# Optimization experiments

Measured on AMD Instinct MI355X. Metric: run time of the kernel, lower is better.

The kernel has to match this reference:

```python
import jax, jax.numpy as jnp
import numpy as np

N, E, G, L = 50000, 800000, 512, 4
DIN, D = 128, 64


def setup_inputs() -> dict:
    key = jax.random.key(0)
    ks = jax.random.split(key, 32)
    s = 0.1  # weight scale
    inp = {
        "nodes_feat": jax.random.normal(ks[0], (N, DIN), jnp.float32),
        "edges_feat": jax.random.normal(ks[1], (E, 1), jnp.float32),
        "nodes_num_norm_sqrt": jax.random.uniform(ks[2], (N, 1), jnp.float32),
        "edges_num_norm_sqrt": jax.random.uniform(ks[3], (E, 1), jnp.float32),
        "W_h": jax.random.normal(ks[4], (DIN, D), jnp.float32) * s,
        "b_h": jax.random.normal(ks[5], (D,), jnp.float32) * s,
        "W_e": jax.random.normal(ks[6], (1, D), jnp.float32) * s,
        "b_e": jax.random.normal(ks[7], (D,), jnp.float32) * s,
        "Wa": jax.random.normal(ks[8], (L, D, D), jnp.float32) * s,
        "ba": jax.random.normal(ks[9], (L, D), jnp.float32) * s,
        "Wb": jax.random.normal(ks[10], (L, D, D), jnp.float32) * s,
        "bb": jax.random.normal(ks[11], (L, D), jnp.float32) * s,
        "Wc": jax.random.normal(ks[12], (L, D, D), jnp.float32) * s,
        "bc": jax.random.normal(ks[13], (L, D), jnp.float32) * s,
        "Wd": jax.random.normal(ks[14], (L, D, D), jnp.float32) * s,
        "bd": jax.random.normal(ks[15], (L, D), jnp.float32) * s,
        "We": jax.random.normal(ks[16], (L, D, D), jnp.float32) * s,
        "be": jax.random.normal(ks[17], (L, D), jnp.float32) * s,
        "gamma_h": jnp.ones((L, D), jnp.float32),
        "beta_h": jnp.zeros((L, D), jnp.float32),
        "gamma_e": jnp.ones((L, D), jnp.float32),
        "beta_e": jnp.zeros((L, D), jnp.float32),
        "edge_src": jax.random.randint(ks[18], (E,), 0, N, jnp.int32),
        "edge_dst": jax.random.randint(ks[19], (E,), 0, N, jnp.int32),
        "node_graph_ids": jnp.sort(jax.random.randint(ks[20], (N,), 0, G, jnp.int32)),
        "num_graphs": G,
    }
    return inp


def _bn(x, gamma, beta):
    # BatchNorm1d, training mode (biased batch statistics)
    mu = jnp.mean(x, axis=0)
    var = jnp.var(x, axis=0)
    return gamma * (x - mu) * jax.lax.rsqrt(var + 1e-5) + beta


def reference(nodes_feat, edges_feat, nodes_num_norm_sqrt, edges_num_norm_sqrt,
              W_h, b_h, W_e, b_e,
              Wa, ba, Wb, bb, Wc, bc, Wd, bd, We, be,
              gamma_h, beta_h, gamma_e, beta_e,
              edge_src, edge_dst, node_graph_ids, num_graphs):
    seg = jax.ops.segment_sum
    n_nodes = nodes_feat.shape[0]
    h = nodes_feat @ W_h + b_h          # [N, D]
    e = edges_feat @ W_e + b_e          # [E, D]
    for l in range(Wa.shape[0]):
        h_in, e_in = h, e
        Ah = h @ Wa[l] + ba[l]
        Bh = h @ Wb[l] + bb[l]
        Dh = h @ Wd[l] + bd[l]
        Eh = h @ We[l] + be[l]
        e_new = (e @ Wc[l] + bc[l]) + Dh[edge_src] + Eh[edge_dst]   # [E, D]
        sigma = jax.nn.sigmoid(e_new)
        num = seg(sigma * Bh[edge_src], edge_dst, num_segments=n_nodes)
        den = seg(sigma, edge_dst, num_segments=n_nodes)
        h_new = Ah + num / (den + 1e-6)
        h_new = h_new * nodes_num_norm_sqrt      # graph norm
        e_new = e_new * edges_num_norm_sqrt
        h_new = jax.nn.relu(_bn(h_new, gamma_h[l], beta_h[l]))
        e_new = jax.nn.relu(_bn(e_new, gamma_e[l], beta_e[l]))
        h = h_in + h_new                          # residual
        e = e_in + e_new
    # dgl.mean_nodes: segment mean of node features per graph
    ones = jnp.ones((n_nodes, 1), h.dtype)
    counts = seg(ones, node_graph_ids, num_segments=num_graphs)
    hg = seg(h, node_graph_ids, num_segments=num_graphs) / jnp.maximum(counts, 1.0)
    return hg
```

## Files before the change

kernel.cpp:

```cpp
#include <hip/hip_runtime.h>
#include <cstddef>

#define DIN 128
#define DD 64

typedef unsigned short bfu;
typedef __attribute__((ext_vector_type(8))) short bf16x8;
typedef __attribute__((ext_vector_type(4))) float f32x4;

static __device__ __forceinline__ float bf2f(bfu u) {
    union { unsigned int i; float f; } v; v.i = ((unsigned int)u) << 16; return v.f;
}
static __device__ __forceinline__ bfu f2bf(float f) {
    union { float f; unsigned int i; } v; v.f = f;
    unsigned int r = v.i + 0x7FFFu + ((v.i >> 16) & 1u);
    return (bfu)(r >> 16);
}
static __device__ __forceinline__ float4 bf4_to_f4(ushort4 u) {
    return make_float4(bf2f(u.x), bf2f(u.y), bf2f(u.z), bf2f(u.w));
}
static __device__ __forceinline__ ushort4 f4_to_bf4(float4 f) {
    ushort4 u; u.x = f2bf(f.x); u.y = f2bf(f.y); u.z = f2bf(f.z); u.w = f2bf(f.w); return u;
}
static __device__ __forceinline__ float sigmoidf_(float x) {
    return 1.0f / (1.0f + __expf(-x));
}
static __device__ __forceinline__ float readlane_f(float v, int lane) {
    return __uint_as_float(__builtin_amdgcn_readlane(__float_as_uint(v), lane));
}

__global__ __launch_bounds__(256) void embed_h_v8(
    const float* __restrict__ x, const float* __restrict__ Wh,
    const float* __restrict__ bh, float* __restrict__ h, int N)
{
    __shared__ float w[DIN][DD];
    __shared__ float xs[32][DIN];
    for (int i = threadIdx.x; i < DIN * DD / 4; i += 256)
        ((float4*)w)[i] = ((const float4*)Wh)[i];
    int row0 = blockIdx.x * 32;
    for (int i = threadIdx.x; i < 32 * DIN / 4; i += 256) {
        int r = i >> 5, k = (i & 31) * 4;
        int row = row0 + r;
        float4 v = make_float4(0.f, 0.f, 0.f, 0.f);
        if (row < N) v = *(const float4*)(x + (size_t)row * DIN + k);
        *(float4*)(&xs[r][k]) = v;
    }
    __syncthreads();
    int rl = threadIdx.x >> 6;
    int c  = threadIdx.x & 63;
    float b = bh[c];
    for (int rr = 0; rr < 8; ++rr) {
        int r = rl * 8 + rr;
        int row = row0 + r;
        if (row >= N) break;
        float acc = b;
        #pragma unroll
        for (int k = 0; k < DIN; k += 4) {
            float4 xv = *(const float4*)(&xs[r][k]);
            acc += xv.x * w[k][c] + xv.y * w[k+1][c] + xv.z * w[k+2][c] + xv.w * w[k+3][c];
        }
        h[(size_t)row * DD + c] = acc;
    }
}

__global__ void csr_hist_v8(const int* __restrict__ dst, int* __restrict__ counts, int E)
{
    for (int i = blockIdx.x * blockDim.x + threadIdx.x; i < E; i += gridDim.x * blockDim.x)
        atomicAdd(&counts[dst[i]], 1);
}

__global__ void csr_scan_a_v8(const int* __restrict__ counts, int* __restrict__ part,
                              int M, int CH)
{
    __shared__ int sd[256];
    int b = blockIdx.x, t = threadIdx.x;
    int idx = b * CH + t;
    int v = (t < CH && idx < M) ? counts[idx] : 0;
    sd[t] = v; __syncthreads();
    for (int off = 128; off > 0; off >>= 1) {
        if (t < off) sd[t] += sd[t + off];
        __syncthreads();
    }
    if (t == 0) part[b] = sd[0];
}

__global__ void csr_scan_b_v8(int* __restrict__ part)
{
    __shared__ int sd[256];
    int t = threadIdx.x;
    int v = part[t];
    sd[t] = v; __syncthreads();
    for (int off = 1; off < 256; off <<= 1) {
        int u = (t >= off) ? sd[t - off] : 0;
        __syncthreads();
        sd[t] += u;
        __syncthreads();
    }
    part[t] = sd[t] - v;
}

__global__ void csr_scan_c_v8(const int* __restrict__ counts, const int* __restrict__ part,
                              int* __restrict__ offsets, int* __restrict__ cursor,
                              int M, int CH)
{
    __shared__ int sd[256];
    int b = blockIdx.x, t = threadIdx.x;
    int idx = b * CH + t;
    int v = (t < CH && idx < M) ? counts[idx] : 0;
    sd[t] = v; __syncthreads();
    for (int off = 1; off < 256; off <<= 1) {
        int u = (t >= off) ? sd[t - off] : 0;
        __syncthreads();
        sd[t] += u;
        __syncthreads();
    }
    int excl = sd[t] - v + part[b];
    if (t < CH && idx < M) { offsets[idx] = excl; cursor[idx] = excl; }
}

__global__ void csr_scatter_v8(const int* __restrict__ dst, int* __restrict__ cursor,
                               int* __restrict__ csr_eid, int E)
{
    for (int i = blockIdx.x * blockDim.x + threadIdx.x; i < E; i += gridDim.x * blockDim.x) {
        int p = atomicAdd(&cursor[dst[i]], 1);
        csr_eid[p] = i;
    }
}

__global__ void perm_build_v8(const int* __restrict__ csr_eid, const int* __restrict__ esrc,
                              const float* __restrict__ enorm,
                              unsigned short* __restrict__ src_p,
                              float* __restrict__ enorm_p, int E)
{
    for (int i = blockIdx.x * blockDim.x + threadIdx.x; i < E; i += gridDim.x * blockDim.x) {
        int eid = csr_eid[i];
        src_p[i] = (unsigned short)esrc[eid];
        enorm_p[i] = enorm[eid];
    }
}

__global__ __launch_bounds__(256) void embed_e_perm_v8(
    const float* __restrict__ ef, const float* __restrict__ We,
    const float* __restrict__ be, const int* __restrict__ csr_eid,
    bfu* __restrict__ e, int E)
{
    int c = (threadIdx.x & 15) * 4;
    float4 w = *(const float4*)(We + c);
    float4 b = *(const float4*)(be + c);
    int total = E * 16;
    int stride = gridDim.x * blockDim.x;
    for (int u = blockIdx.x * blockDim.x + threadIdx.x; u < total; u += stride) {
        int j = u >> 4;
        float f = ef[csr_eid[j]];
        float4 o;
        o.x = f * w.x + b.x; o.y = f * w.y + b.y;
        o.z = f * w.z + b.z; o.w = f * w.w + b.w;
        *(ushort4*)(e + (size_t)j * DD + c) = f4_to_bf4(o);
    }
}

__global__ __launch_bounds__(192) void node_mm3_v8(
    const float* __restrict__ h,
    const float* __restrict__ Wa, const float* __restrict__ ba,
    const float* __restrict__ Wb, const float* __restrict__ bbv,
    const float* __restrict__ Wd, const float* __restrict__ bd,
    bfu* __restrict__ Ah, bfu* __restrict__ DBh, int N)
{
    __shared__ float hs[64][DD];
    int row0 = blockIdx.x * 64;
    for (int i = threadIdx.x; i < 64 * 16; i += 192) {
        int r = i >> 4, cc = (i & 15) * 4;
        int row = row0 + r;
        float4 v = make_float4(0.f, 0.f, 0.f, 0.f);
        if (row < N) v = *(const float4*)(h + (size_t)row * DD + cc);
        *(float4*)(&hs[r][cc]) = v;
    }
    __syncthreads();
    int m = threadIdx.x / 64;
    int c = threadIdx.x & 63;
    const float* W    = (m == 0) ? Wa : (m == 1) ? Wb : Wd;
    const float* bias = (m == 0) ? ba : (m == 1) ? bbv : bd;
    float wcol[DD];
    #pragma unroll
    for (int k = 0; k < DD; ++k) wcol[k] = W[k * DD + c];
    float b = bias[c];
    int rmax = (N - row0 < 64) ? (N - row0) : 64;
    for (int r = 0; r < rmax; ++r) {
        float acc = b;
        #pragma unroll
        for (int k = 0; k < DD; k += 4) {
            float4 hv = *(const float4*)(&hs[r][k]);
            acc += hv.x * wcol[k] + hv.y * wcol[k+1] + hv.z * wcol[k+2] + hv.w * wcol[k+3];
        }
        bfu o = f2bf(acc);
        size_t row = (size_t)(row0 + r);
        if (m == 0)      Ah[row * DD + c] = o;
        else if (m == 1) DBh[row * 128 + 2 * c + 1] = o;
        else             DBh[row * 128 + 2 * c] = o;
    }
}

__global__ __launch_bounds__(256) void ec_gemm_v8(
    bfu* __restrict__ e, bfu* __restrict__ ecs,
    const float* __restrict__ Wc, const float* __restrict__ bc,
    const float* __restrict__ bnp, const float* __restrict__ gamma,
    const float* __restrict__ beta, int apply, int store_e, int E)
{
    __shared__ bfu els[64 * 72];
    int l  = threadIdx.x & 63;
    int w  = threadIdx.x >> 6;
    int lr = l & 15;
    int ld = l >> 4;

    bf16x8 bfrag[4][2];
    #pragma unroll
    for (int ct = 0; ct < 4; ++ct)
        #pragma unroll
        for (int kh = 0; kh < 2; ++kh)
            #pragma unroll
            for (int j = 0; j < 8; ++j)
                bfrag[ct][kh][j] = (short)f2bf(Wc[(kh * 32 + 8 * ld + j) * DD + ct * 16 + lr]);

    float bcl[4];
    #pragma unroll
    for (int ct = 0; ct < 4; ++ct) bcl[ct] = bc[ct * 16 + lr];

    int sr  = threadIdx.x >> 4;
    int scg = threadIdx.x & 15;
    float4 mu = make_float4(0,0,0,0), isd = mu, g4 = mu, bt = mu;
    if (apply) {
        mu  = *(const float4*)(bnp + scg * 4);
        isd = *(const float4*)(bnp + DD + scg * 4);
        g4  = *(const float4*)(gamma + scg * 4);
        bt  = *(const float4*)(beta + scg * 4);
    }

    int stride = gridDim.x * 64;
    for (int base = blockIdx.x * 64; base < E; base += stride) {
        __syncthreads();
        #pragma unroll
        for (int rr = 0; rr < 4; ++rr) {
            int r = rr * 16 + sr;
            int j = base + r;
            if (j < E) {
                size_t off = (size_t)j * DD + scg * 4;
                ushort4 raw = *(const ushort4*)(e + off);
                if (apply) {
                    float4 v = bf4_to_f4(raw);
                    float4 es4 = bf4_to_f4(*(const ushort4*)(ecs + off));
                    v.x += fmaxf(g4.x * (es4.x - mu.x) * isd.x + bt.x, 0.f);
                    v.y += fmaxf(g4.y * (es4.y - mu.y) * isd.y + bt.y, 0.f);
                    v.z += fmaxf(g4.z * (es4.z - mu.z) * isd.z + bt.z, 0.f);
                    v.w += fmaxf(g4.w * (es4.w - mu.w) * isd.w + bt.w, 0.f);
                    ushort4 nb = f4_to_bf4(v);
                    if (store_e) *(ushort4*)(e + off) = nb;
                    *(ushort4*)(&els[r * 72 + scg * 4]) = nb;
                } else {
                    *(ushort4*)(&els[r * 72 + scg * 4]) = raw;
                }
            }
        }
        __syncthreads();
        bf16x8 a0 = *(const bf16x8*)(&els[(w * 16 + lr) * 72 + 8 * ld]);
        bf16x8 a1 = *(const bf16x8*)(&els[(w * 16 + lr) * 72 + 32 + 8 * ld]);
        #pragma unroll
        for (int ct = 0; ct < 4; ++ct) {
            f32x4 acc = {0.f, 0.f, 0.f, 0.f};
            acc = __builtin_amdgcn_mfma_f32_16x16x32_bf16(a0, bfrag[ct][0], acc, 0, 0, 0);
            acc = __builtin_amdgcn_mfma_f32_16x16x32_bf16(a1, bfrag[ct][1], acc, 0, 0, 0);
            #pragma unroll
            for (int j = 0; j < 4; ++j) {
                int row = base + w * 16 + 4 * ld + j;
                if (row < E)
                    ecs[(size_t)row * DD + ct * 16 + lr] = f2bf(acc[j] + bcl[ct]);
            }
        }
    }
}

__global__ __launch_bounds__(256) void fused_accum_v8(
    bfu* __restrict__ ecs,
    const bfu* __restrict__ Ah, const bfu* __restrict__ DBh,
    const float* __restrict__ h, const float* __restrict__ We, const float* __restrict__ be,
    const int* __restrict__ coffs, const unsigned short* __restrict__ src_p,
    const float* __restrict__ enorm_p, const float* __restrict__ nnorm,
    float* __restrict__ hraw, float* __restrict__ stats, int N, int store_es)
{
    __shared__ float red[4][4][DD];
    int wid = threadIdx.x >> 6;
    int c   = threadIdx.x & 63;
    float wcol[DD];
    #pragma unroll
    for (int k = 0; k < DD; ++k) wcol[k] = We[k * DD + c];
    float bec = be[c];
    float se = 0.f, se2 = 0.f, sh = 0.f, sh2 = 0.f;

    int gw = blockIdx.x * 4 + wid;
    int gstride = gridDim.x * 4;
    for (int n = gw; n < N; n += gstride) {
        int j0 = coffs[n], j1 = coffs[n + 1];
        float hv = h[(size_t)n * DD + c];
        float e0 = bec, e1 = 0.f, e2 = 0.f, e3 = 0.f;
        #pragma unroll
        for (int k = 0; k < DD; k += 4) {
            e0 += readlane_f(hv, k)     * wcol[k];
            e1 += readlane_f(hv, k + 1) * wcol[k + 1];
            e2 += readlane_f(hv, k + 2) * wcol[k + 2];
            e3 += readlane_f(hv, k + 3) * wcol[k + 3];
        }
        float ehv = (e0 + e1) + (e2 + e3);
        float num = 0.f, den = 0.f;
        for (int j = j0; j < j1; ++j) {
            int s = src_p[j];
            float en = enorm_p[j];
            ushort2 db = *(const ushort2*)(DBh + (size_t)s * 128 + 2 * c);
            float er = bf2f(ecs[(size_t)j * DD + c]) + bf2f(db.x) + ehv;
            float sg = sigmoidf_(er);
            num += sg * bf2f(db.y);
            den += sg;
            float es = er * en;
            if (store_es) ecs[(size_t)j * DD + c] = f2bf(es);
            se += es; se2 += es * es;
        }
        float x = (bf2f(Ah[(size_t)n * DD + c]) + num / (den + 1e-6f)) * nnorm[n];
        hraw[(size_t)n * DD + c] = x;
        sh += x; sh2 += x * x;
    }

    red[wid][0][c] = se;  red[wid][1][c] = se2;
    red[wid][2][c] = sh;  red[wid][3][c] = sh2;
    __syncthreads();
    if (threadIdx.x < DD) {
        int t = threadIdx.x;
        float t0 = 0.f, t1 = 0.f, t2 = 0.f, t3 = 0.f;
        #pragma unroll
        for (int w = 0; w < 4; ++w) {
            t0 += red[w][0][t]; t1 += red[w][1][t];
            t2 += red[w][2][t]; t3 += red[w][3][t];
        }
        unsafeAtomicAdd(&stats[t], t0);
        unsafeAtomicAdd(&stats[DD + t], t1);
        unsafeAtomicAdd(&stats[2 * DD + t], t2);
        unsafeAtomicAdd(&stats[3 * DD + t], t3);
    }
}

__global__ void bn_fin2_v8(const float* __restrict__ stats, float Ecnt, float Ncnt,
                           float* __restrict__ bnp)
{
    int t = threadIdx.x;
    if (t < DD) {
        float mu  = stats[t] / Ecnt;
        float var = stats[DD + t] / Ecnt - mu * mu;
        bnp[t] = mu;
        bnp[DD + t] = rsqrtf(var + 1e-5f);
    } else {
        int cc = t - DD;
        float mu  = stats[2 * DD + cc] / Ncnt;
        float var = stats[3 * DD + cc] / Ncnt - mu * mu;
        bnp[2 * DD + cc] = mu;
        bnp[3 * DD + cc] = rsqrtf(var + 1e-5f);
    }
}

__global__ __launch_bounds__(256) void node_apply_v8(
    const float* __restrict__ hraw, const float* __restrict__ bnph,
    const float* __restrict__ gamma, const float* __restrict__ beta,
    float* __restrict__ h, int N)
{
    int cc = (threadIdx.x & 15) * 4;
    float4 mu = *(const float4*)(bnph + cc);
    float4 is = *(const float4*)(bnph + DD + cc);
    float4 g  = *(const float4*)(gamma + cc);
    float4 b  = *(const float4*)(beta + cc);
    int total = N * 16;
    int stride = gridDim.x * blockDim.x;
    for (int u = blockIdx.x * blockDim.x + threadIdx.x; u < total; u += stride) {
        size_t off = ((size_t)(u >> 4)) * DD + ((u & 15) * 4);
        float4 x   = *(const float4*)(hraw + off);
        float4 hin = *(const float4*)(h + off);
        float4 y;
        y.x = hin.x + fmaxf(g.x * (x.x - mu.x) * is.x + b.x, 0.f);
        y.y = hin.y + fmaxf(g.y * (x.y - mu.y) * is.y + b.y, 0.f);
        y.z = hin.z + fmaxf(g.z * (x.z - mu.z) * is.z + b.z, 0.f);
        y.w = hin.w + fmaxf(g.w * (x.w - mu.w) * is.w + b.w, 0.f);
        *(float4*)(h + off) = y;
    }
}

__global__ __launch_bounds__(256) void readout_v8(
    const float* __restrict__ h, const int* __restrict__ gid,
    float* __restrict__ hg, float* __restrict__ counts, int N)
{
    int total = N * 16;
    int stride = gridDim.x * blockDim.x;
    for (int u = blockIdx.x * blockDim.x + threadIdx.x; u < total; u += stride) {
        int n = u >> 4;
        int c = (u & 15) * 4;
        int g = gid[n];
        float4 x = *(const float4*)(h + (size_t)n * DD + c);
        float* p = hg + (size_t)g * DD + c;
        unsafeAtomicAdd(p + 0, x.x);
        unsafeAtomicAdd(p + 1, x.y);
        unsafeAtomicAdd(p + 2, x.z);
        unsafeAtomicAdd(p + 3, x.w);
        if ((u & 15) == 0) unsafeAtomicAdd(&counts[g], 1.0f);
    }
}

__global__ void readout_div_v8(const float* __restrict__ hg,
                               const float* __restrict__ counts,
                               float* __restrict__ out, int GD)
{
    int i = blockIdx.x * blockDim.x + threadIdx.x;
    if (i < GD) {
        int g = i >> 6;
        out[i] = hg[i] / fmaxf(counts[g], 1.0f);
    }
}

extern "C" void kernel_launch(void* const* d_in, const int* in_sizes, int n_in,
                              void* d_out, int out_size, void* d_ws, size_t ws_size,
                              hipStream_t stream)
{
    const float* nodes_feat = (const float*)d_in[0];
    const float* edges_feat = (const float*)d_in[1];
    const float* nnorm      = (const float*)d_in[2];
    const float* enorm      = (const float*)d_in[3];
    const float* W_h = (const float*)d_in[4];
    const float* b_h = (const float*)d_in[5];
    const float* W_e = (const float*)d_in[6];
    const float* b_e = (const float*)d_in[7];
    const float* Wa  = (const float*)d_in[8];
    const float* ba  = (const float*)d_in[9];
    const float* Wb_ = (const float*)d_in[10];
    const float* bb_ = (const float*)d_in[11];
    const float* Wc  = (const float*)d_in[12];
    const float* bc  = (const float*)d_in[13];
    const float* Wd  = (const float*)d_in[14];
    const float* bd  = (const float*)d_in[15];
    const float* We_ = (const float*)d_in[16];
    const float* be_ = (const float*)d_in[17];
    const float* gamma_h = (const float*)d_in[18];
    const float* beta_h  = (const float*)d_in[19];
    const float* gamma_e = (const float*)d_in[20];
    const float* beta_e  = (const float*)d_in[21];
    const int* esrc = (const int*)d_in[22];
    const int* edst = (const int*)d_in[23];
    const int* gid  = (const int*)d_in[24];

    const int N = in_sizes[0] / DIN;
    const int E = in_sizes[1];
    const int G = out_size / DD;
    const int L = in_sizes[8] / (DD * DD);

    float* f = (float*)d_ws;
    float* h       = f; f += (size_t)N * DD;
    float* hraw    = f; f += (size_t)N * DD;
    float* stats   = f; f += 256;
    float* bnp     = f; f += 256;
    float* hg      = f; f += (size_t)G * DD;
    float* gcnt    = f; f += G;
    int*   coffs   = (int*)f; f += (size_t)(N + 2);
    float* enorm_p = f; f += (size_t)E;
    unsigned short* src_p = (unsigned short*)f; f += (size_t)((E + 1) / 2);
    bfu* bp = (bfu*)f;
    bfu* Ah  = bp; bp += (size_t)N * DD;
    bfu* DBh = bp; bp += (size_t)N * 128;
    bfu* e_p = bp; bp += (size_t)E * DD;
    bfu* ecs = bp; bp += (size_t)E * DD;
    int* ccounts = (int*)ecs;
    int* ccursor = ccounts + (N + 1);
    int* cpart   = ccursor + (N + 1);
    int* csr_eid = cpart + 256;

    dim3 blk(256);

    hipMemsetAsync(hg, 0, ((size_t)G * DD + G) * sizeof(float), stream);
    hipMemsetAsync(ccounts, 0, (size_t)(N + 1) * sizeof(int), stream);

    embed_h_v8<<<(N + 31) / 32, blk, 0, stream>>>(nodes_feat, W_h, b_h, h, N);

    const int M  = N + 1;
    const int CH = (M + 255) / 256;
    csr_hist_v8<<<2048, blk, 0, stream>>>(edst, ccounts, E);
    csr_scan_a_v8<<<256, blk, 0, stream>>>(ccounts, cpart, M, CH);
    csr_scan_b_v8<<<1, blk, 0, stream>>>(cpart);
    csr_scan_c_v8<<<256, blk, 0, stream>>>(ccounts, cpart, coffs, ccursor, M, CH);
    csr_scatter_v8<<<2048, blk, 0, stream>>>(edst, ccursor, csr_eid, E);
    perm_build_v8<<<2048, blk, 0, stream>>>(csr_eid, esrc, enorm, src_p, enorm_p, E);
    embed_e_perm_v8<<<2048, blk, 0, stream>>>(edges_feat, W_e, b_e, csr_eid, e_p, E);

    for (int l = 0; l < L; ++l) {
        node_mm3_v8<<<(N + 63) / 64, dim3(192), 0, stream>>>(
            h, Wa + (size_t)l * DD * DD, ba + (size_t)l * DD,
            Wb_ + (size_t)l * DD * DD, bb_ + (size_t)l * DD,
            Wd + (size_t)l * DD * DD, bd + (size_t)l * DD,
            Ah, DBh, N);
        hipMemsetAsync(stats, 0, 256 * sizeof(float), stream);
        ec_gemm_v8<<<2048, blk, 0, stream>>>(
            e_p, ecs, Wc + (size_t)l * DD * DD, bc + (size_t)l * DD,
            bnp,
            (l > 0) ? gamma_e + (size_t)(l - 1) * DD : gamma_e,
            (l > 0) ? beta_e  + (size_t)(l - 1) * DD : beta_e,
            (l > 0) ? 1 : 0,
            (l < L - 1) ? 1 : 0, E);
        fused_accum_v8<<<2048, blk, 0, stream>>>(
            ecs, Ah, DBh, h,
            We_ + (size_t)l * DD * DD, be_ + (size_t)l * DD,
            coffs, src_p, enorm_p, nnorm, hraw, stats, N,
            (l < L - 1) ? 1 : 0);
        bn_fin2_v8<<<1, 128, 0, stream>>>(stats, (float)E, (float)N, bnp);
        node_apply_v8<<<1024, blk, 0, stream>>>(
            hraw, bnp + 2 * DD,
            gamma_h + (size_t)l * DD, beta_h + (size_t)l * DD, h, N);
    }

    readout_v8<<<1024, blk, 0, stream>>>(h, gid, hg, gcnt, N);
    readout_div_v8<<<(G * DD + 255) / 256, blk, 0, stream>>>(
        hg, gcnt, (float*)d_out, G * DD);
}
```

Before: 1.554 ms.

## Move Eh GEMM into node kernel, drop LDS staging in edge GEMM, fold BN affine

The node GEMM kernel now computes four projections, including the Eh = h@We term that the edge-accumulate kernel used to recompute per node with readlane reductions. It also writes Ah in fp32 straight into the hraw buffer so the accumulate kernel can update it in place. The edge GEMM loads MFMA fragments directly from global memory instead of staging through LDS with block barriers. BatchNorm is folded into precomputed per-channel scale and shift, and the edge accumulation loop is unrolled by two to expose more memory-level parallelism. The cost is an extra Eh buffer round trip through memory and bf16 rounding of Eh.

```diff
diff --git a/kernel.cpp b/kernel.cpp
--- a/kernel.cpp
+++ b/kernel.cpp
@@ -25,11 +25,8 @@
 static __device__ __forceinline__ float sigmoidf_(float x) {
     return 1.0f / (1.0f + __expf(-x));
 }
-static __device__ __forceinline__ float readlane_f(float v, int lane) {
-    return __uint_as_float(__builtin_amdgcn_readlane(__float_as_uint(v), lane));
-}
-
-__global__ __launch_bounds__(256) void embed_h_v8(
+
+__global__ __launch_bounds__(256) void embed_h_v9(
     const float* __restrict__ x, const float* __restrict__ Wh,
     const float* __restrict__ bh, float* __restrict__ h, int N)
 {
@@ -63,13 +60,13 @@
     }
 }
 
-__global__ void csr_hist_v8(const int* __restrict__ dst, int* __restrict__ counts, int E)
+__global__ void csr_hist_v9(const int* __restrict__ dst, int* __restrict__ counts, int E)
 {
     for (int i = blockIdx.x * blockDim.x + threadIdx.x; i < E; i += gridDim.x * blockDim.x)
         atomicAdd(&counts[dst[i]], 1);
 }
 
-__global__ void csr_scan_a_v8(const int* __restrict__ counts, int* __restrict__ part,
+__global__ void csr_scan_a_v9(const int* __restrict__ counts, int* __restrict__ part,
                               int M, int CH)
 {
     __shared__ int sd[256];
@@ -84,7 +81,7 @@
     if (t == 0) part[b] = sd[0];
 }
 
-__global__ void csr_scan_b_v8(int* __restrict__ part)
+__global__ void csr_scan_b_v9(int* __restrict__ part)
 {
     __shared__ int sd[256];
     int t = threadIdx.x;
@@ -99,7 +96,7 @@
     part[t] = sd[t] - v;
 }
 
-__global__ void csr_scan_c_v8(const int* __restrict__ counts, const int* __restrict__ part,
+__global__ void csr_scan_c_v9(const int* __restrict__ counts, const int* __restrict__ part,
                               int* __restrict__ offsets, int* __restrict__ cursor,
                               int M, int CH)
 {
@@ -118,7 +115,7 @@
     if (t < CH && idx < M) { offsets[idx] = excl; cursor[idx] = excl; }
 }
 
-__global__ void csr_scatter_v8(const int* __restrict__ dst, int* __restrict__ cursor,
+__global__ void csr_scatter_v9(const int* __restrict__ dst, int* __restrict__ cursor,
                                int* __restrict__ csr_eid, int E)
 {
     for (int i = blockIdx.x * blockDim.x + threadIdx.x; i < E; i += gridDim.x * blockDim.x) {
@@ -127,7 +124,7 @@
     }
 }
 
-__global__ void perm_build_v8(const int* __restrict__ csr_eid, const int* __restrict__ esrc,
+__global__ void perm_build_v9(const int* __restrict__ csr_eid, const int* __restrict__ esrc,
                               const float* __restrict__ enorm,
                               unsigned short* __restrict__ src_p,
                               float* __restrict__ enorm_p, int E)
@@ -139,7 +136,7 @@
     }
 }
 
-__global__ __launch_bounds__(256) void embed_e_perm_v8(
+__global__ __launch_bounds__(256) void embed_e_perm_v9(
     const float* __restrict__ ef, const float* __restrict__ We,
     const float* __restrict__ be, const int* __restrict__ csr_eid,
     bfu* __restrict__ e, int E)
@@ -159,16 +156,17 @@
     }
 }
 
-__global__ __launch_bounds__(192) void node_mm3_v8(
+__global__ __launch_bounds__(256) void node_mm4_v9(
     const float* __restrict__ h,
     const float* __restrict__ Wa, const float* __restrict__ ba,
     const float* __restrict__ Wb, const float* __restrict__ bbv,
     const float* __restrict__ Wd, const float* __restrict__ bd,
-    bfu* __restrict__ Ah, bfu* __restrict__ DBh, int N)
+    const float* __restrict__ We, const float* __restrict__ be,
+    float* __restrict__ hrawA, bfu* __restrict__ DBh, bfu* __restrict__ Eh, int N)
 {
     __shared__ float hs[64][DD];
     int row0 = blockIdx.x * 64;
-    for (int i = threadIdx.x; i < 64 * 16; i += 192) {
+    for (int i = threadIdx.x; i < 64 * 16; i += 256) {
         int r = i >> 4, cc = (i & 15) * 4;
         int row = row0 + r;
         float4 v = make_float4(0.f, 0.f, 0.f, 0.f);
@@ -176,10 +174,10 @@
         *(float4*)(&hs[r][cc]) = v;
     }
     __syncthreads();
-    int m = threadIdx.x / 64;
+    int m = threadIdx.x >> 6;
     int c = threadIdx.x & 63;
-    const float* W    = (m == 0) ? Wa : (m == 1) ? Wb : Wd;
-    const float* bias = (m == 0) ? ba : (m == 1) ? bbv : bd;
+    const float* W    = (m == 0) ? Wa : (m == 1) ? Wb : (m == 2) ? Wd : We;
+    const float* bias = (m == 0) ? ba : (m == 1) ? bbv : (m == 2) ? bd : be;
     float wcol[DD];
     #pragma unroll
     for (int k = 0; k < DD; ++k) wcol[k] = W[k * DD + c];
@@ -192,23 +190,21 @@
             float4 hv = *(const float4*)(&hs[r][k]);
             acc += hv.x * wcol[k] + hv.y * wcol[k+1] + hv.z * wcol[k+2] + hv.w * wcol[k+3];
         }
-        bfu o = f2bf(acc);
         size_t row = (size_t)(row0 + r);
-        if (m == 0)      Ah[row * DD + c] = o;
-        else if (m == 1) DBh[row * 128 + 2 * c + 1] = o;
-        else             DBh[row * 128 + 2 * c] = o;
-    }
-}
-
-__global__ __launch_bounds__(256) void ec_gemm_v8(
+        if (m == 0)      hrawA[row * DD + c] = acc;
+        else if (m == 1) DBh[row * 128 + 2 * c + 1] = f2bf(acc);
+        else if (m == 2) DBh[row * 128 + 2 * c] = f2bf(acc);
+        else             Eh[row * DD + c] = f2bf(acc);
+    }
+}
+
+__global__ __launch_bounds__(256) void ec_gemm_v9(
     bfu* __restrict__ e, bfu* __restrict__ ecs,
     const float* __restrict__ Wc, const float* __restrict__ bc,
-    const float* __restrict__ bnp, const float* __restrict__ gamma,
-    const float* __restrict__ beta, int apply, int store_e, int E)
-{
-    __shared__ bfu els[64 * 72];
+    const float* __restrict__ bnAB,
+    int apply, int store_e, int E)
+{
     int l  = threadIdx.x & 63;
-    int w  = threadIdx.x >> 6;
     int lr = l & 15;
     int ld = l >> 4;
 
@@ -225,44 +221,45 @@
     #pragma unroll
     for (int ct = 0; ct < 4; ++ct) bcl[ct] = bc[ct * 16 + lr];
 
-    int sr  = threadIdx.x >> 4;
-    int scg = threadIdx.x & 15;
-    float4 mu = make_float4(0,0,0,0), isd = mu, g4 = mu, bt = mu;
+    float A0[8], B0[8], A1[8], B1[8];
     if (apply) {
-        mu  = *(const float4*)(bnp + scg * 4);
-        isd = *(const float4*)(bnp + DD + scg * 4);
-        g4  = *(const float4*)(gamma + scg * 4);
-        bt  = *(const float4*)(beta + scg * 4);
-    }
-
-    int stride = gridDim.x * 64;
-    for (int base = blockIdx.x * 64; base < E; base += stride) {
-        __syncthreads();
         #pragma unroll
-        for (int rr = 0; rr < 4; ++rr) {
-            int r = rr * 16 + sr;
-            int j = base + r;
-            if (j < E) {
-                size_t off = (size_t)j * DD + scg * 4;
-                ushort4 raw = *(const ushort4*)(e + off);
-                if (apply) {
-                    float4 v = bf4_to_f4(raw);
-                    float4 es4 = bf4_to_f4(*(const ushort4*)(ecs + off));
-                    v.x += fmaxf(g4.x * (es4.x - mu.x) * isd.x + bt.x, 0.f);
-                    v.y += fmaxf(g4.y * (es4.y - mu.y) * isd.y + bt.y, 0.f);
-                    v.z += fmaxf(g4.z * (es4.z - mu.z) * isd.z + bt.z, 0.f);
-                    v.w += fmaxf(g4.w * (es4.w - mu.w) * isd.w + bt.w, 0.f);
-                    ushort4 nb = f4_to_bf4(v);
-                    if (store_e) *(ushort4*)(e + off) = nb;
-                    *(ushort4*)(&els[r * 72 + scg * 4]) = nb;
-                } else {
-                    *(ushort4*)(&els[r * 72 + scg * 4]) = raw;
+        for (int j = 0; j < 8; ++j) {
+            A0[j] = bnAB[8 * ld + j];
+            B0[j] = bnAB[64 + 8 * ld + j];
+            A1[j] = bnAB[32 + 8 * ld + j];
+            B1[j] = bnAB[64 + 32 + 8 * ld + j];
+        }
+    }
+
+    int wg = blockIdx.x * 4 + (threadIdx.x >> 6);
+    int nw = gridDim.x * 4;
+    for (int base = wg * 16; base < E; base += nw * 16) {
+        int row = base + lr;
+        bf16x8 a0 = {0, 0, 0, 0, 0, 0, 0, 0};
+        bf16x8 a1 = {0, 0, 0, 0, 0, 0, 0, 0};
+        if (row < E) {
+            size_t off = (size_t)row * DD + 8 * ld;
+            bf16x8 r0 = *(const bf16x8*)(e + off);
+            bf16x8 r1 = *(const bf16x8*)(e + off + 32);
+            if (apply) {
+                bf16x8 s0 = *(const bf16x8*)(ecs + off);
+                bf16x8 s1 = *(const bf16x8*)(ecs + off + 32);
+                #pragma unroll
+                for (int j = 0; j < 8; ++j) {
+                    float v0 = bf2f((bfu)r0[j]) + fmaxf(A0[j] * bf2f((bfu)s0[j]) + B0[j], 0.f);
+                    float v1 = bf2f((bfu)r1[j]) + fmaxf(A1[j] * bf2f((bfu)s1[j]) + B1[j], 0.f);
+                    a0[j] = (short)f2bf(v0);
+                    a1[j] = (short)f2bf(v1);
                 }
+                if (store_e) {
+                    *(bf16x8*)(e + off) = a0;
+                    *(bf16x8*)(e + off + 32) = a1;
+                }
+            } else {
+                a0 = r0; a1 = r1;
             }
         }
-        __syncthreads();
-        bf16x8 a0 = *(const bf16x8*)(&els[(w * 16 + lr) * 72 + 8 * ld]);
-        bf16x8 a1 = *(const bf16x8*)(&els[(w * 16 + lr) * 72 + 32 + 8 * ld]);
         #pragma unroll
         for (int ct = 0; ct < 4; ++ct) {
             f32x4 acc = {0.f, 0.f, 0.f, 0.f};
@@ -270,65 +267,75 @@
             acc = __builtin_amdgcn_mfma_f32_16x16x32_bf16(a1, bfrag[ct][1], acc, 0, 0, 0);
             #pragma unroll
             for (int j = 0; j < 4; ++j) {
-                int row = base + w * 16 + 4 * ld + j;
-                if (row < E)
-                    ecs[(size_t)row * DD + ct * 16 + lr] = f2bf(acc[j] + bcl[ct]);
+                int orow = base + 4 * ld + j;
+                if (orow < E)
+                    ecs[(size_t)orow * DD + ct * 16 + lr] = f2bf(acc[j] + bcl[ct]);
             }
         }
     }
 }
 
-__global__ __launch_bounds__(256) void fused_accum_v8(
-    bfu* __restrict__ ecs,
-    const bfu* __restrict__ Ah, const bfu* __restrict__ DBh,
-    const float* __restrict__ h, const float* __restrict__ We, const float* __restrict__ be,
+__global__ __launch_bounds__(256) void fused_accum_v9(
+    bfu* __restrict__ ecs, float* __restrict__ hrawA,
+    const bfu* __restrict__ DBh, const bfu* __restrict__ Eh,
     const int* __restrict__ coffs, const unsigned short* __restrict__ src_p,
     const float* __restrict__ enorm_p, const float* __restrict__ nnorm,
-    float* __restrict__ hraw, float* __restrict__ stats, int N, int store_es)
+    float* __restrict__ stats, int N, int store_es)
 {
     __shared__ float red[4][4][DD];
     int wid = threadIdx.x >> 6;
     int c   = threadIdx.x & 63;
-    float wcol[DD];
-    #pragma unroll
-    for (int k = 0; k < DD; ++k) wcol[k] = We[k * DD + c];
-    float bec = be[c];
-    float se = 0.f, se2 = 0.f, sh = 0.f, sh2 = 0.f;
+    float se0 = 0.f, se20 = 0.f, se1 = 0.f, se21 = 0.f;
+    float sh = 0.f, sh2 = 0.f;
 
     int gw = blockIdx.x * 4 + wid;
     int gstride = gridDim.x * 4;
     for (int n = gw; n < N; n += gstride) {
         int j0 = coffs[n], j1 = coffs[n + 1];
-        float hv = h[(size_t)n * DD + c];
-        float e0 = bec, e1 = 0.f, e2 = 0.f, e3 = 0.f;
-        #pragma unroll
-        for (int k = 0; k < DD; k += 4) {
-            e0 += readlane_f(hv, k)     * wcol[k];
-            e1 += readlane_f(hv, k + 1) * wcol[k + 1];
-            e2 += readlane_f(hv, k + 2) * wcol[k + 2];
-            e3 += readlane_f(hv, k + 3) * wcol[k + 3];
-        }
-        float ehv = (e0 + e1) + (e2 + e3);
-        float num = 0.f, den = 0.f;
-        for (int j = j0; j < j1; ++j) {
-            int s = src_p[j];
-            float en = enorm_p[j];
-            ushort2 db = *(const ushort2*)(DBh + (size_t)s * 128 + 2 * c);
-            float er = bf2f(ecs[(size_t)j * DD + c]) + bf2f(db.x) + ehv;
-            float sg = sigmoidf_(er);
-            num += sg * bf2f(db.y);
-            den += sg;
-            float es = er * en;
-            if (store_es) ecs[(size_t)j * DD + c] = f2bf(es);
-            se += es; se2 += es * es;
-        }
-        float x = (bf2f(Ah[(size_t)n * DD + c]) + num / (den + 1e-6f)) * nnorm[n];
-        hraw[(size_t)n * DD + c] = x;
+        float ehv = bf2f(Eh[(size_t)n * DD + c]);
+        float a = hrawA[(size_t)n * DD + c];
+        float num0 = 0.f, den0 = 0.f, num1 = 0.f, den1 = 0.f;
+        int j = j0;
+        for (; j + 1 < j1; j += 2) {
+            int s0 = src_p[j], s1 = src_p[j + 1];
+            float en0 = enorm_p[j], en1 = enorm_p[j + 1];
+            bfu ec0 = ecs[(size_t)j * DD + c];
+            bfu ec1 = ecs[(size_t)(j + 1) * DD + c];
+            ushort2 db0 = *(const ushort2*)(DBh + (size_t)s0 * 128 + 2 * c);
+            ushort2 db1 = *(const ushort2*)(DBh + (size_t)s1 * 128 + 2 * c);
+            float er0 = bf2f(ec0) + bf2f(db0.x) + ehv;
+            float er1 = bf2f(ec1) + bf2f(db1.x) + ehv;
+            float sg0 = sigmoidf_(er0);
+            float sg1 = sigmoidf_(er1);
+            num0 += sg0 * bf2f(db0.y); den0 += sg0;
+            num1 += sg1 * bf2f(db1.y); den1 += sg1;
+            float es0 = er0 * en0, es1 = er1 * en1;
+            if (store_es) {
+                ecs[(size_t)j * DD + c] = f2bf(es0);
+                ecs[(size_t)(j + 1) * DD + c] = f2bf(es1);
+            }
+            se0 += es0; se20 += es0 * es0;
+            se1 += es1; se21 += es1 * es1;
+        }
+        if (j < j1) {
+            int s0 = src_p[j];
+            float en0 = enorm_p[j];
+            bfu ec0 = ecs[(size_t)j * DD + c];
+            ushort2 db0 = *(const ushort2*)(DBh + (size_t)s0 * 128 + 2 * c);
+            float er0 = bf2f(ec0) + bf2f(db0.x) + ehv;
+            float sg0 = sigmoidf_(er0);
+            num0 += sg0 * bf2f(db0.y); den0 += sg0;
+            float es0 = er0 * en0;
+            if (store_es) ecs[(size_t)j * DD + c] = f2bf(es0);
+            se0 += es0; se20 += es0 * es0;
+        }
+        float x = (a + (num0 + num1) / ((den0 + den1) + 1e-6f)) * nnorm[n];
+        hrawA[(size_t)n * DD + c] = x;
         sh += x; sh2 += x * x;
     }
 
-    red[wid][0][c] = se;  red[wid][1][c] = se2;
-    red[wid][2][c] = sh;  red[wid][3][c] = sh2;
+    red[wid][0][c] = se0 + se1;  red[wid][1][c] = se20 + se21;
+    red[wid][2][c] = sh;         red[wid][3][c] = sh2;
     __syncthreads();
     if (threadIdx.x < DD) {
         int t = threadIdx.x;
@@ -345,50 +352,51 @@
     }
 }
 
-__global__ void bn_fin2_v8(const float* __restrict__ stats, float Ecnt, float Ncnt,
-                           float* __restrict__ bnp)
+__global__ void bn_fin2_v9(const float* __restrict__ stats, float Ecnt, float Ncnt,
+                           const float* __restrict__ gamma_e, const float* __restrict__ beta_e,
+                           const float* __restrict__ gamma_h, const float* __restrict__ beta_h,
+                           float* __restrict__ bnAB)
 {
     int t = threadIdx.x;
     if (t < DD) {
         float mu  = stats[t] / Ecnt;
         float var = stats[DD + t] / Ecnt - mu * mu;
-        bnp[t] = mu;
-        bnp[DD + t] = rsqrtf(var + 1e-5f);
+        float A = gamma_e[t] * rsqrtf(var + 1e-5f);
+        bnAB[t] = A;
+        bnAB[DD + t] = beta_e[t] - A * mu;
     } else {
         int cc = t - DD;
         float mu  = stats[2 * DD + cc] / Ncnt;
         float var = stats[3 * DD + cc] / Ncnt - mu * mu;
-        bnp[2 * DD + cc] = mu;
-        bnp[3 * DD + cc] = rsqrtf(var + 1e-5f);
-    }
-}
-
-__global__ __launch_bounds__(256) void node_apply_v8(
-    const float* __restrict__ hraw, const float* __restrict__ bnph,
-    const float* __restrict__ gamma, const float* __restrict__ beta,
+        float A = gamma_h[cc] * rsqrtf(var + 1e-5f);
+        bnAB[2 * DD + cc] = A;
+        bnAB[3 * DD + cc] = beta_h[cc] - A * mu;
+    }
+}
+
+__global__ __launch_bounds__(256) void node_apply_v9(
+    const float* __restrict__ hrawA, const float* __restrict__ bnAB,
     float* __restrict__ h, int N)
 {
     int cc = (threadIdx.x & 15) * 4;
-    float4 mu = *(const float4*)(bnph + cc);
-    float4 is = *(const float4*)(bnph + DD + cc);
-    float4 g  = *(const float4*)(gamma + cc);
-    float4 b  = *(const float4*)(beta + cc);
+    float4 A = *(const float4*)(bnAB + 2 * DD + cc);
+    float4 B = *(const float4*)(bnAB + 3 * DD + cc);
     int total = N * 16;
     int stride = gridDim.x * blockDim.x;
     for (int u = blockIdx.x * blockDim.x + threadIdx.x; u < total; u += stride) {
         size_t off = ((size_t)(u >> 4)) * DD + ((u & 15) * 4);
-        float4 x   = *(const float4*)(hraw + off);
+        float4 x   = *(const float4*)(hrawA + off);
         float4 hin = *(const float4*)(h + off);
         float4 y;
-        y.x = hin.x + fmaxf(g.x * (x.x - mu.x) * is.x + b.x, 0.f);
-        y.y = hin.y + fmaxf(g.y * (x.y - mu.y) * is.y + b.y, 0.f);
-        y.z = hin.z + fmaxf(g.z * (x.z - mu.z) * is.z + b.z, 0.f);
-        y.w = hin.w + fmaxf(g.w * (x.w - mu.w) * is.w + b.w, 0.f);
+        y.x = hin.x + fmaxf(A.x * x.x + B.x, 0.f);
+        y.y = hin.y + fmaxf(A.y * x.y + B.y, 0.f);
+        y.z = hin.z + fmaxf(A.z * x.z + B.z, 0.f);
+        y.w = hin.w + fmaxf(A.w * x.w + B.w, 0.f);
         *(float4*)(h + off) = y;
     }
 }
 
-__global__ __launch_bounds__(256) void readout_v8(
+__global__ __launch_bounds__(256) void readout_v9(
     const float* __restrict__ h, const int* __restrict__ gid,
     float* __restrict__ hg, float* __restrict__ counts, int N)
 {
@@ -408,7 +416,7 @@
     }
 }
 
-__global__ void readout_div_v8(const float* __restrict__ hg,
+__global__ void readout_div_v9(const float* __restrict__ hg,
                                const float* __restrict__ counts,
                                float* __restrict__ out, int GD)
 {
@@ -456,17 +464,17 @@
 
     float* f = (float*)d_ws;
     float* h       = f; f += (size_t)N * DD;
-    float* hraw    = f; f += (size_t)N * DD;
+    float* hrawA   = f; f += (size_t)N * DD;
     float* stats   = f; f += 256;
-    float* bnp     = f; f += 256;
+    float* bnAB    = f; f += 256;
     float* hg      = f; f += (size_t)G * DD;
     float* gcnt    = f; f += G;
     int*   coffs   = (int*)f; f += (size_t)(N + 2);
     float* enorm_p = f; f += (size_t)E;
     unsigned short* src_p = (unsigned short*)f; f += (size_t)((E + 1) / 2);
     bfu* bp = (bfu*)f;
-    bfu* Ah  = bp; bp += (size_t)N * DD;
     bfu* DBh = bp; bp += (size_t)N * 128;
+    bfu* Eh  = bp; bp += (size_t)N * DD;
     bfu* e_p = bp; bp += (size_t)E * DD;
     bfu* ecs = bp; bp += (size_t)E * DD;
     int* ccounts = (int*)ecs;
@@ -479,44 +487,43 @@
     hipMemsetAsync(hg, 0, ((size_t)G * DD + G) * sizeof(float), stream);
     hipMemsetAsync(ccounts, 0, (size_t)(N + 1) * sizeof(int), stream);
 
-    embed_h_v8<<<(N + 31) / 32, blk, 0, stream>>>(nodes_feat, W_h, b_h, h, N);
+    embed_h_v9<<<(N + 31) / 32, blk, 0, stream>>>(nodes_feat, W_h, b_h, h, N);
 
     const int M  = N + 1;
     const int CH = (M + 255) / 256;
-    csr_hist_v8<<<2048, blk, 0, stream>>>(edst, ccounts, E);
-    csr_scan_a_v8<<<256, blk, 0, stream>>>(ccounts, cpart, M, CH);
-    csr_scan_b_v8<<<1, blk, 0, stream>>>(cpart);
-    csr_scan_c_v8<<<256, blk, 0, stream>>>(ccounts, cpart, coffs, ccursor, M, CH);
-    csr_scatter_v8<<<2048, blk, 0, stream>>>(edst, ccursor, csr_eid, E);
-    perm_build_v8<<<2048, blk, 0, stream>>>(csr_eid, esrc, enorm, src_p, enorm_p, E);
-    embed_e_perm_v8<<<2048, blk, 0, stream>>>(edges_feat, W_e, b_e, csr_eid, e_p, E);
+    csr_hist_v9<<<2048, blk, 0, stream>>>(edst, ccounts, E);
+    csr_scan_a_v9<<<256, blk, 0, stream>>>(ccounts, cpart, M, CH);
+    csr_scan_b_v9<<<1, blk, 0, stream>>>(cpart);
+    csr_scan_c_v9<<<256, blk, 0, stream>>>(ccounts, cpart, coffs, ccursor, M, CH);
+    csr_scatter_v9<<<2048, blk, 0, stream>>>(edst, ccursor, csr_eid, E);
+    perm_build_v9<<<2048, blk, 0, stream>>>(csr_eid, esrc, enorm, src_p, enorm_p, E);
+    embed_e_perm_v9<<<2048, blk, 0, stream>>>(edges_feat, W_e, b_e, csr_eid, e_p, E);
 
     for (int l = 0; l < L; ++l) {
-        node_mm3_v8<<<(N + 63) / 64, dim3(192), 0, stream>>>(
+        node_mm4_v9<<<(N + 63) / 64, blk, 0, stream>>>(
             h, Wa + (size_t)l * DD * DD, ba + (size_t)l * DD,
             Wb_ + (size_t)l * DD * DD, bb_ + (size_t)l * DD,
             Wd + (size_t)l * DD * DD, bd + (size_t)l * DD,
-            Ah, DBh, N);
+            We_ + (size_t)l * DD * DD, be_ + (size_t)l * DD,
+            hrawA, DBh, Eh, N);
         hipMemsetAsync(stats, 0, 256 * sizeof(float), stream);
-        ec_gemm_v8<<<2048, blk, 0, stream>>>(
+        ec_gemm_v9<<<2048, blk, 0, stream>>>(
             e_p, ecs, Wc + (size_t)l * DD * DD, bc + (size_t)l * DD,
-            bnp,
-            (l > 0) ? gamma_e + (size_t)(l - 1) * DD : gamma_e,
-            (l > 0) ? beta_e  + (size_t)(l - 1) * DD : beta_e,
+            bnAB,
             (l > 0) ? 1 : 0,
             (l < L - 1) ? 1 : 0, E);
-        fused_accum_v8<<<2048, blk, 0, stream>>>(
-            ecs, Ah, DBh, h,
-            We_ + (size_t)l * DD * DD, be_ + (size_t)l * DD,
-            coffs, src_p, enorm_p, nnorm, hraw, stats, N,
+        fused_accum_v9<<<2048, blk, 0, stream>>>(
+            ecs, hrawA, DBh, Eh,
+            coffs, src_p, enorm_p, nnorm, stats, N,
             (l < L - 1) ? 1 : 0);
-        bn_fin2_v8<<<1, 128, 0, stream>>>(stats, (float)E, (float)N, bnp);
-        node_apply_v8<<<1024, blk, 0, stream>>>(
-            hraw, bnp + 2 * DD,
-            gamma_h + (size_t)l * DD, beta_h + (size_t)l * DD, h, N);
-    }
-
-    readout_v8<<<1024, blk, 0, stream>>>(h, gid, hg, gcnt, N);
-    readout_div_v8<<<(G * DD + 255) / 256, blk, 0, stream>>>(
+        bn_fin2_v9<<<1, 128, 0, stream>>>(
+            stats, (float)E, (float)N,
+            gamma_e + (size_t)l * DD, beta_e + (size_t)l * DD,
+            gamma_h + (size_t)l * DD, beta_h + (size_t)l * DD, bnAB);
+        node_apply_v9<<<1024, blk, 0, stream>>>(hrawA, bnAB, h, N);
+    }
+
+    readout_v9<<<1024, blk, 0, stream>>>(h, gid, hg, gcnt, N);
+    readout_div_v9<<<(G * DD + 255) / 256, blk, 0, stream>>>(
         hg, gcnt, (float*)d_out, G * DD);
 }
```

Result: faster. 1.305 ms (-16.0%).
